# Kernel tuning notes

Hardware: AMD Instinct MI355X
Metric: run time of the kernel (lower is better)

## Reference

```python
import jax, jax.numpy as jnp
import numpy as np

N_EXPERTS = 8
TOPK = 2
D_MODEL = 1024
D_FF = 4096

def setup_inputs() -> dict:
    key = jax.random.key(0)
    k_x, k_g, k_1, k_2 = jax.random.split(key, 4)
    x = jax.random.normal(k_x, (4, 2048, D_MODEL), dtype=jnp.float32)
    Wg = jax.random.normal(k_g, (D_MODEL, N_EXPERTS), dtype=jnp.float32) * 0.02
    W1 = jax.random.normal(k_1, (N_EXPERTS, D_MODEL, D_FF), dtype=jnp.float32) * 0.02
    W2 = jax.random.normal(k_2, (N_EXPERTS, D_FF, D_MODEL), dtype=jnp.float32) * 0.02
    return {"x": x, "Wg": Wg, "W1": W1, "W2": W2}

def reference(x, Wg, W1, W2):
    B, S, D = x.shape
    xt = x.reshape(-1, D)                      # [T, D]
    T = xt.shape[0]
    logits = xt @ Wg                            # [T, E]
    vals, idx = jax.lax.top_k(logits, TOPK)     # [T, K]
    w = jax.nn.softmax(vals, axis=-1)           # renormalize over selected experts
    # scatter top-k weights into dense [T, E] gate matrix (zeros elsewhere)
    gates = jnp.zeros((T, N_EXPERTS), dtype=x.dtype).at[jnp.arange(T)[:, None], idx].set(w)
    out = jnp.zeros_like(xt)
    for e in range(N_EXPERTS):                  # fixed small loop over experts
        h = jax.nn.silu(xt @ W1[e]) @ W2[e]     # [T, D]
        out = out + gates[:, e:e+1] * h
    return out.reshape(B, S, D)
```

## Files before the change

kernel.cpp:

```cpp
#include <hip/hip_runtime.h>
#include <hip/hip_bf16.h>
#include <math.h>

#define T_TOK 8192
#define DM 1024
#define DF 4096
#define NE 8
#define MAXT 72

typedef __attribute__((ext_vector_type(4))) float  f32x4;
typedef __attribute__((ext_vector_type(8))) short  s16x8;
typedef __attribute__((ext_vector_type(8))) unsigned short u16x8;
typedef __attribute__((ext_vector_type(4))) unsigned short u16x4;

__device__ __forceinline__ unsigned short f2bf(float f) {
    unsigned int u = __builtin_bit_cast(unsigned int, f);
    u = (u + 0x7FFFu + ((u >> 16) & 1u)) >> 16;
    return (unsigned short)u;
}

#define GLDS16(gptr, lptr)                                                         \
    __builtin_amdgcn_global_load_lds(                                              \
        (const __attribute__((address_space(1))) void*)(gptr),                     \
        (__attribute__((address_space(3))) void*)(lptr), 16, 0, 0)

#define BAR() asm volatile("s_barrier" ::: "memory")

template<int W>
__device__ __forceinline__ void waitvm() {
    if constexpr (W == 6)      asm volatile("s_waitcnt vmcnt(6)" ::: "memory");
    else if constexpr (W == 3) asm volatile("s_waitcnt vmcnt(3)" ::: "memory");
    else                       asm volatile("s_waitcnt vmcnt(0)" ::: "memory");
}

__global__ __launch_bounds__(256) void route_kernel(
    const float* __restrict__ x, const float* __restrict__ Wg,
    int* __restrict__ counts, int* __restrict__ lists, float* __restrict__ pw,
    unsigned short* __restrict__ xb)
{
    int tok  = (int)((blockIdx.x * blockDim.x + threadIdx.x) >> 6);
    int lane = threadIdx.x & 63;
    if (tok >= T_TOK) return;

    const float* xr = x + (size_t)tok * DM;
    float acc[NE];
#pragma unroll
    for (int e = 0; e < NE; ++e) acc[e] = 0.f;

    for (int i = lane; i < DM; i += 64) {
        float xv = xr[i];
        const float* wr = Wg + (size_t)i * NE;
#pragma unroll
        for (int e = 0; e < NE; ++e) acc[e] += xv * wr[e];
    }

    if (xb) {
        unsigned short* xrow = xb + (size_t)tok * DM;
#pragma unroll
        for (int i = lane * 4; i < DM; i += 256) {
            float4 v = *reinterpret_cast<const float4*>(xr + i);
            u16x4 o;
            o[0] = f2bf(v.x); o[1] = f2bf(v.y); o[2] = f2bf(v.z); o[3] = f2bf(v.w);
            *reinterpret_cast<u16x4*>(xrow + i) = o;
        }
    }

#pragma unroll
    for (int e = 0; e < NE; ++e) {
#pragma unroll
        for (int off = 32; off > 0; off >>= 1)
            acc[e] += __shfl_xor(acc[e], off, 64);
    }

    if (lane == 0) {
        int i0 = 0; float v0 = acc[0];
#pragma unroll
        for (int e = 1; e < NE; ++e) if (acc[e] > v0) { v0 = acc[e]; i0 = e; }
        int i1 = -1; float v1 = -INFINITY;
#pragma unroll
        for (int e = 0; e < NE; ++e) if (e != i0 && acc[e] > v1) { v1 = acc[e]; i1 = e; }
        float e1 = __expf(v1 - v0);
        float s  = 1.f + e1;
        int p0 = tok * 2, p1 = tok * 2 + 1;
        pw[p0] = 1.f / s;
        pw[p1] = e1 / s;
        int pos0 = atomicAdd(&counts[i0], 1);
        lists[i0 * T_TOK + pos0] = p0;
        int pos1 = atomicAdd(&counts[i1], 1);
        lists[i1 * T_TOK + pos1] = p1;
    }
}

__global__ void offsets_kernel(const int* __restrict__ counts, int* __restrict__ offsets,
                               unsigned* __restrict__ table, int* __restrict__ ntp)
{
    if (threadIdx.x == 0) {
        int s = 0, ti = 0;
        for (int e = 0; e < NE; ++e) {
            offsets[e] = s;
            int cnt = counts[e];
            for (int t0 = 0; t0 < cnt; t0 += 256)
                table[ti++] = ((unsigned)e << 20) | (unsigned)t0;
            s += cnt;
        }
        ntp[0] = ti;
        for (; ti < MAXT; ++ti) table[ti] = 0xFFFFFFFFu;
    }
}

template<int K, int N>
__global__ __launch_bounds__(256) void transpose_conv_kernel(
    const float* __restrict__ W, unsigned short* __restrict__ Wt)
{
    int e  = blockIdx.z;
    int k0 = blockIdx.x * 64;
    int n0 = blockIdx.y * 64;
    const float* We = W + (size_t)e * K * N;
    unsigned short* Wte = Wt + (size_t)e * K * N;

    __shared__ unsigned short t[64][73];
    int c4 = (threadIdx.x & 15) * 4;
    int r  = threadIdx.x >> 4;
#pragma unroll
    for (int i = 0; i < 4; ++i) {
        int rr = r + i * 16;
        float4 v = *reinterpret_cast<const float4*>(We + (size_t)(k0 + rr) * N + n0 + c4);
        t[rr][c4 + 0] = f2bf(v.x); t[rr][c4 + 1] = f2bf(v.y);
        t[rr][c4 + 2] = f2bf(v.z); t[rr][c4 + 3] = f2bf(v.w);
    }
    __syncthreads();
    int kc = (threadIdx.x & 7) * 8;
    int rn = threadIdx.x >> 3;
#pragma unroll
    for (int i = 0; i < 2; ++i) {
        int nn = rn + i * 32;
        u16x8 o;
#pragma unroll
        for (int j = 0; j < 8; ++j) o[j] = t[kc + j][nn];
        *reinterpret_cast<u16x8*>(Wte + (size_t)(n0 + nn) * K + k0 + kc) = o;
    }
}

template<int N, int K, int SPLITK, bool IS_G1>
__global__ __launch_bounds__(512, 4) void moe_gemm11(
    const unsigned short* __restrict__ A,
    const unsigned short* __restrict__ Wt,
    const int* __restrict__ counts, const int* __restrict__ offsets,
    const int* __restrict__ lists, const unsigned* __restrict__ table,
    const int* __restrict__ ntp, const float* __restrict__ pw,
    unsigned short* __restrict__ Hout, float* __restrict__ Oout)
{
    constexpr int NT  = N / 128;
    constexpr int PAN = NT * SPLITK;
    constexpr int KS  = K / SPLITK;
    constexpr int NC  = KS / 32;
    static_assert(NC >= 4, "pipeline depth");

    __shared__ __attribute__((aligned(16))) char lds[73728];

    int ntl  = ntp[0];
    int live = ntl * PAN;
    int orig = blockIdx.x;
    if (orig >= live) return;
    int q = live >> 3, r = live & 7;
    int xq = orig & 7, ib = orig >> 3;
    int work = (xq < r ? xq * (q + 1) : r * (q + 1) + (xq - r) * q) + ib;
    int rt    = work / PAN;
    int panel = work - rt * PAN;
    int nt    = panel >> (SPLITK - 1);
    int sk    = panel & (SPLITK - 1);
    int koff  = sk * KS;

    unsigned te = table[rt];
    int e     = (int)(te >> 20);
    int slot0 = (int)(te & 0xFFFFFu);
    int cnt   = counts[e];
    int off   = offsets[e];
    int ntile = nt * 128;

    int tid  = threadIdx.x;
    int lane = tid & 63;
    int wid  = tid >> 6;
    int wm = wid >> 1;
    int wn = wid & 1;
    int l15 = lane & 15, l4 = lane >> 4;

    const unsigned short* Be = Wt + (size_t)e * N * K;

    int ssw = ((tid & 3) ^ ((tid >> 3) & 3)) * 8;
    unsigned aOff0, aOff1, bOff;
    {
        int r0 = tid >> 2;
#pragma unroll
        for (int u = 0; u < 2; ++u) {
            int sl = slot0 + u * 128 + r0;
            unsigned grow;
            if (IS_G1) grow = (sl < cnt) ? (unsigned)(lists[e * T_TOK + sl] >> 1) : 0u;
            else       grow = (unsigned)(off + ((sl < cnt) ? sl : slot0));
            unsigned v = grow * (unsigned)K + (unsigned)(koff + ssw);
            if (u == 0) aOff0 = v; else aOff1 = v;
        }
        bOff = (unsigned)(ntile + r0) * (unsigned)K + (unsigned)(koff + ssw);
    }

    auto stage = [&](int s, int c) {
        int ko = c * 32;
        char* dA = lds + s * 16384 + tid * 16;
        char* dB = lds + 49152 + s * 8192 + tid * 16;
        GLDS16(A + aOff0 + ko, dA);
        GLDS16(A + aOff1 + ko, dA + 8192);
        GLDS16(Be + bOff + ko, dB);
    };

    int swzb = (l4 ^ ((l15 >> 1) & 3)) * 16;
    int aRd = (wm * 64 + l15) * 64 + swzb;
    int bRd = (wn * 64 + l15) * 64 + swzb;

    f32x4 acc[4][4];
#pragma unroll
    for (int m = 0; m < 4; ++m)
#pragma unroll
        for (int n = 0; n < 4; ++n) acc[m][n] = (f32x4){0.f, 0.f, 0.f, 0.f};

    auto compute = [&](int s) {
        const char* Ab = lds + s * 16384;
        const char* Bb = lds + 49152 + s * 8192;
        s16x8 af[4];
#pragma unroll
        for (int m = 0; m < 4; ++m)
            af[m] = *reinterpret_cast<const s16x8*>(Ab + aRd + m * 1024);
        __builtin_amdgcn_s_setprio(1);
#pragma unroll
        for (int n = 0; n < 4; ++n) {
            s16x8 bf = *reinterpret_cast<const s16x8*>(Bb + bRd + n * 1024);
#pragma unroll
            for (int m = 0; m < 4; ++m)
                acc[m][n] = __builtin_amdgcn_mfma_f32_16x16x32_bf16(af[m], bf, acc[m][n], 0, 0, 0);
        }
        __builtin_amdgcn_s_setprio(0);
    };

    stage(0, 0); stage(1, 1); stage(2, 2);
    int sslot = 0;
    for (int c = 0; c < NC; ++c) {
        if (c + 2 < NC)      waitvm<6>();
        else if (c + 1 < NC) waitvm<3>();
        else                 waitvm<0>();
        BAR();
        compute(sslot);
        BAR();
        if (c + 3 < NC) stage(sslot, c + 3);
        sslot = (sslot == 2) ? 0 : sslot + 1;
    }

#pragma unroll
    for (int m = 0; m < 4; ++m) {
        int trow = wm * 64 + m * 16 + l4 * 4;
#pragma unroll
        for (int rr = 0; rr < 4; ++rr) {
            int slot = slot0 + trow + rr;
            if (slot >= cnt) continue;
            if (IS_G1) {
                unsigned short* hr = Hout + (size_t)(off + slot) * N;
#pragma unroll
                for (int n = 0; n < 4; ++n) {
                    int col = ntile + wn * 64 + n * 16 + l15;
                    float v = acc[m][n][rr];
                    float s = v / (1.f + __expf(-v));
                    hr[col] = f2bf(s);
                }
            } else {
                int p = lists[e * T_TOK + slot];
                float w = pw[p];
                float* orow = Oout + (size_t)(p >> 1) * DM;
#pragma unroll
                for (int n = 0; n < 4; ++n) {
                    int col = ntile + wn * 64 + n * 16 + l15;
                    atomicAdd(orow + col, w * acc[m][n][rr]);
                }
            }
        }
    }
}

#define BMF 16
#define BFF 256
__global__ __launch_bounds__(256) void expert_gemm_f32(
    const float* __restrict__ x, const float* __restrict__ W1, const float* __restrict__ W2,
    const int* __restrict__ counts, const int* __restrict__ lists, const float* __restrict__ pw,
    float* __restrict__ out)
{
    int e    = blockIdx.y;
    int tile = blockIdx.x;
    int cnt  = counts[e];
    int start = tile * BMF;
    if (start >= cnt) return;

    __shared__ float xs[BMF][DM];
    __shared__ float hs[BMF][BFF];
    __shared__ int   toks[BMF];
    __shared__ float wgt[BMF];

    int tid = threadIdx.x;
    int nm  = cnt - start; if (nm > BMF) nm = BMF;

    if (tid < BMF) {
        if (tid < nm) {
            int p = lists[e * T_TOK + start + tid];
            toks[tid] = p >> 1;
            wgt[tid]  = pw[p];
        } else { toks[tid] = -1; wgt[tid] = 0.f; }
    }
    __syncthreads();
    for (int m = 0; m < BMF; ++m) {
        int t = toks[m];
        const float* xr = (t >= 0) ? (x + (size_t)t * DM) : nullptr;
        for (int i = tid; i < DM; i += 256) xs[m][i] = (t >= 0) ? xr[i] : 0.f;
    }
    __syncthreads();

    const float* W1e = W1 + (size_t)e * DM * DF;
    const float* W2e = W2 + (size_t)e * DF * DM;
    float acc[BMF][4];
#pragma unroll
    for (int m = 0; m < BMF; ++m)
#pragma unroll
        for (int c = 0; c < 4; ++c) acc[m][c] = 0.f;

    for (int fc = 0; fc < DF; fc += BFF) {
        float hacc[BMF];
#pragma unroll
        for (int m = 0; m < BMF; ++m) hacc[m] = 0.f;
        const float* w1col = W1e + fc + tid;
#pragma unroll 4
        for (int i = 0; i < DM; ++i) {
            float w1v = w1col[(size_t)i * DF];
#pragma unroll
            for (int m = 0; m < BMF; ++m) hacc[m] += xs[m][i] * w1v;
        }
        __syncthreads();
#pragma unroll
        for (int m = 0; m < BMF; ++m) {
            float v = hacc[m];
            hs[m][tid] = v / (1.f + __expf(-v));
        }
        __syncthreads();
        const float* w2base = W2e + (size_t)fc * DM + tid * 4;
        for (int f = 0; f < BFF; ++f) {
            float4 w2v = *reinterpret_cast<const float4*>(w2base + (size_t)f * DM);
#pragma unroll
            for (int m = 0; m < BMF; ++m) {
                float h = hs[m][f];
                acc[m][0] += h * w2v.x; acc[m][1] += h * w2v.y;
                acc[m][2] += h * w2v.z; acc[m][3] += h * w2v.w;
            }
        }
        __syncthreads();
    }
    int c0 = tid * 4;
#pragma unroll
    for (int m = 0; m < BMF; ++m) {
        int t = toks[m];
        if (t < 0) continue;
        float w = wgt[m];
        float* op = out + (size_t)t * DM + c0;
        atomicAdd(op + 0, w * acc[m][0]);
        atomicAdd(op + 1, w * acc[m][1]);
        atomicAdd(op + 2, w * acc[m][2]);
        atomicAdd(op + 3, w * acc[m][3]);
    }
}

extern "C" void kernel_launch(void* const* d_in, const int* in_sizes, int n_in,
                              void* d_out, int out_size, void* d_ws, size_t ws_size,
                              hipStream_t stream)
{
    const float* x  = (const float*)d_in[0];
    const float* Wg = (const float*)d_in[1];
    const float* W1 = (const float*)d_in[2];
    const float* W2 = (const float*)d_in[3];
    float* out = (float*)d_out;

    char* ws = (char*)d_ws;
    int*      counts  = (int*)(ws + 0);
    int*      offsets = (int*)(ws + 64);
    int*      ntp     = (int*)(ws + 128);
    unsigned* table   = (unsigned*)(ws + 256);
    int*      lists   = (int*)(ws + 2048);
    float*    pw      = (float*)(ws + 2048 + 262144);

    const size_t o_xb  = 524288;
    const size_t sz_xb = (size_t)T_TOK * DM * 2;
    const size_t o_w1t = o_xb + sz_xb;
    const size_t sz_w  = (size_t)NE * DM * DF * 2;
    const size_t o_w2t = o_w1t + sz_w;
    const size_t o_h   = o_w2t + sz_w;
    const size_t sz_h  = (size_t)(2 * T_TOK) * DF * 2;
    const size_t NEEDED = o_h + sz_h;

    bool fast = (ws_size >= NEEDED);
    unsigned short* xb = fast ? (unsigned short*)(ws + o_xb) : nullptr;

    hipMemsetAsync(counts, 0, 64, stream);
    route_kernel<<<T_TOK / 4, 256, 0, stream>>>(x, Wg, counts, lists, pw, xb);

    if (fast) {
        unsigned short* w1t = (unsigned short*)(ws + o_w1t);
        unsigned short* w2t = (unsigned short*)(ws + o_w2t);
        unsigned short* H   = (unsigned short*)(ws + o_h);

        hipMemsetAsync(d_out, 0, (size_t)out_size * sizeof(float), stream);
        offsets_kernel<<<1, 64, 0, stream>>>(counts, offsets, table, ntp);
        {
            dim3 g(DM / 64, DF / 64, NE);
            transpose_conv_kernel<DM, DF><<<g, 256, 0, stream>>>(W1, w1t);
        }
        {
            dim3 g(DF / 64, DM / 64, NE);
            transpose_conv_kernel<DF, DM><<<g, 256, 0, stream>>>(W2, w2t);
        }
        moe_gemm11<DF, DM, 1, true><<<dim3(MAXT * 32), 512, 0, stream>>>(
            xb, w1t, counts, offsets, lists, table, ntp, pw, H, nullptr);
        moe_gemm11<DM, DF, 2, false><<<dim3(MAXT * 16), 512, 0, stream>>>(
            H, w2t, counts, offsets, lists, table, ntp, pw, nullptr, out);
    } else {
        hipMemsetAsync(d_out, 0, (size_t)out_size * sizeof(float), stream);
        dim3 grid(T_TOK / BMF, NE);
        expert_gemm_f32<<<grid, 256, 0, stream>>>(x, W1, W2, counts, lists, pw, out);
    }
}
```

Baseline: 695.3 us.

## Fold output zeroing into routing, merge transposes, compute expert tiles in GEMM

Zeroes the output buffer inside the routing kernel instead of a separate memset, merges the two weight transpose/convert kernels into one launch, and removes the offsets kernel by having each GEMM block rebuild the tile table from the expert counts. The routing dot product is also vectorized with float4 loads, reusing the x loads for the bf16 conversion. This cuts several launches and a redundant pass over x, in exchange for a small amount of redundant per-block scalar work in the GEMMs.

```diff
diff --git a/kernel.cpp b/kernel.cpp
--- a/kernel.cpp
+++ b/kernel.cpp
@@ -36,31 +36,45 @@
 __global__ __launch_bounds__(256) void route_kernel(
     const float* __restrict__ x, const float* __restrict__ Wg,
     int* __restrict__ counts, int* __restrict__ lists, float* __restrict__ pw,
-    unsigned short* __restrict__ xb)
+    unsigned short* __restrict__ xb, float* __restrict__ outz)
 {
+    {
+        size_t base = ((size_t)blockIdx.x * 256 + threadIdx.x) * 16;
+        float4 z = {0.f, 0.f, 0.f, 0.f};
+#pragma unroll
+        for (int j = 0; j < 4; ++j)
+            *reinterpret_cast<float4*>(outz + base + j * 4) = z;
+    }
+
     int tok  = (int)((blockIdx.x * blockDim.x + threadIdx.x) >> 6);
     int lane = threadIdx.x & 63;
     if (tok >= T_TOK) return;
 
     const float* xr = x + (size_t)tok * DM;
+    unsigned short* xrow = xb ? (xb + (size_t)tok * DM) : nullptr;
+
     float acc[NE];
 #pragma unroll
     for (int e = 0; e < NE; ++e) acc[e] = 0.f;
 
-    for (int i = lane; i < DM; i += 64) {
-        float xv = xr[i];
-        const float* wr = Wg + (size_t)i * NE;
-#pragma unroll
-        for (int e = 0; e < NE; ++e) acc[e] += xv * wr[e];
-    }
-
-    if (xb) {
-        unsigned short* xrow = xb + (size_t)tok * DM;
-#pragma unroll
-        for (int i = lane * 4; i < DM; i += 256) {
-            float4 v = *reinterpret_cast<const float4*>(xr + i);
+#pragma unroll
+    for (int s = 0; s < 4; ++s) {
+        int i = s * 256 + lane * 4;
+        float4 xv = *reinterpret_cast<const float4*>(xr + i);
+#pragma unroll
+        for (int j = 0; j < 4; ++j) {
+            const float* wr = Wg + (size_t)(i + j) * NE;
+            float4 w0 = *reinterpret_cast<const float4*>(wr);
+            float4 w1 = *reinterpret_cast<const float4*>(wr + 4);
+            float xs = (j == 0) ? xv.x : (j == 1) ? xv.y : (j == 2) ? xv.z : xv.w;
+            acc[0] += xs * w0.x; acc[1] += xs * w0.y;
+            acc[2] += xs * w0.z; acc[3] += xs * w0.w;
+            acc[4] += xs * w1.x; acc[5] += xs * w1.y;
+            acc[6] += xs * w1.z; acc[7] += xs * w1.w;
+        }
+        if (xrow) {
             u16x4 o;
-            o[0] = f2bf(v.x); o[1] = f2bf(v.y); o[2] = f2bf(v.z); o[3] = f2bf(v.w);
+            o[0] = f2bf(xv.x); o[1] = f2bf(xv.y); o[2] = f2bf(xv.z); o[3] = f2bf(xv.w);
             *reinterpret_cast<u16x4*>(xrow + i) = o;
         }
     }
@@ -91,39 +105,31 @@
     }
 }
 
-__global__ void offsets_kernel(const int* __restrict__ counts, int* __restrict__ offsets,
-                               unsigned* __restrict__ table, int* __restrict__ ntp)
+__global__ __launch_bounds__(256) void transpose_conv_all(
+    const float* __restrict__ W1, const float* __restrict__ W2,
+    unsigned short* __restrict__ w1t, unsigned short* __restrict__ w2t)
 {
-    if (threadIdx.x == 0) {
-        int s = 0, ti = 0;
-        for (int e = 0; e < NE; ++e) {
-            offsets[e] = s;
-            int cnt = counts[e];
-            for (int t0 = 0; t0 < cnt; t0 += 256)
-                table[ti++] = ((unsigned)e << 20) | (unsigned)t0;
-            s += cnt;
-        }
-        ntp[0] = ti;
-        for (; ti < MAXT; ++ti) table[ti] = 0xFFFFFFFFu;
-    }
-}
-
-template<int K, int N>
-__global__ __launch_bounds__(256) void transpose_conv_kernel(
-    const float* __restrict__ W, unsigned short* __restrict__ Wt)
-{
-    int e  = blockIdx.z;
-    int k0 = blockIdx.x * 64;
-    int n0 = blockIdx.y * 64;
+    int id = blockIdx.x;
+    const float* W; unsigned short* Wt; int K, N, e, k0, n0;
+    if (id < 8192) {
+        W = W1; Wt = w1t; K = DM; N = DF;
+        e = id >> 10; int r = id & 1023;
+        k0 = (r & 15) * 64; n0 = (r >> 4) * 64;
+    } else {
+        id -= 8192;
+        W = W2; Wt = w2t; K = DF; N = DM;
+        e = id >> 10; int r = id & 1023;
+        k0 = (r >> 4) * 64; n0 = (r & 15) * 64;
+    }
     const float* We = W + (size_t)e * K * N;
     unsigned short* Wte = Wt + (size_t)e * K * N;
 
     __shared__ unsigned short t[64][73];
     int c4 = (threadIdx.x & 15) * 4;
-    int r  = threadIdx.x >> 4;
+    int rr0 = threadIdx.x >> 4;
 #pragma unroll
     for (int i = 0; i < 4; ++i) {
-        int rr = r + i * 16;
+        int rr = rr0 + i * 16;
         float4 v = *reinterpret_cast<const float4*>(We + (size_t)(k0 + rr) * N + n0 + c4);
         t[rr][c4 + 0] = f2bf(v.x); t[rr][c4 + 1] = f2bf(v.y);
         t[rr][c4 + 2] = f2bf(v.z); t[rr][c4 + 3] = f2bf(v.w);
@@ -142,12 +148,11 @@
 }
 
 template<int N, int K, int SPLITK, bool IS_G1>
-__global__ __launch_bounds__(512, 4) void moe_gemm11(
+__global__ __launch_bounds__(512, 4) void moe_gemm14(
     const unsigned short* __restrict__ A,
     const unsigned short* __restrict__ Wt,
-    const int* __restrict__ counts, const int* __restrict__ offsets,
-    const int* __restrict__ lists, const unsigned* __restrict__ table,
-    const int* __restrict__ ntp, const float* __restrict__ pw,
+    const int* __restrict__ counts, const int* __restrict__ lists,
+    const float* __restrict__ pw,
     unsigned short* __restrict__ Hout, float* __restrict__ Oout)
 {
     constexpr int NT  = N / 128;
@@ -158,7 +163,13 @@
 
     __shared__ __attribute__((aligned(16))) char lds[73728];
 
-    int ntl  = ntp[0];
+    int cnts[NE];
+#pragma unroll
+    for (int i = 0; i < NE; ++i) cnts[i] = counts[i];
+    int ntl = 0;
+#pragma unroll
+    for (int i = 0; i < NE; ++i) ntl += (cnts[i] + 255) >> 8;
+
     int live = ntl * PAN;
     int orig = blockIdx.x;
     if (orig >= live) return;
@@ -171,11 +182,17 @@
     int sk    = panel & (SPLITK - 1);
     int koff  = sk * KS;
 
-    unsigned te = table[rt];
-    int e     = (int)(te >> 20);
-    int slot0 = (int)(te & 0xFFFFFu);
-    int cnt   = counts[e];
-    int off   = offsets[e];
+    int e = 0, tb = 0, off = 0, cnt = 0;
+    {
+        int ctb = 0, cob = 0; bool found = false;
+#pragma unroll
+        for (int i = 0; i < NE; ++i) {
+            int ti = (cnts[i] + 255) >> 8;
+            if (!found && rt < ctb + ti) { e = i; tb = ctb; off = cob; cnt = cnts[i]; found = true; }
+            ctb += ti; cob += cnts[i];
+        }
+    }
+    int slot0 = (rt - tb) << 8;
     int ntile = nt * 128;
 
     int tid  = threadIdx.x;
@@ -383,9 +400,6 @@
 
     char* ws = (char*)d_ws;
     int*      counts  = (int*)(ws + 0);
-    int*      offsets = (int*)(ws + 64);
-    int*      ntp     = (int*)(ws + 128);
-    unsigned* table   = (unsigned*)(ws + 256);
     int*      lists   = (int*)(ws + 2048);
     float*    pw      = (float*)(ws + 2048 + 262144);
 
@@ -402,29 +416,19 @@
     unsigned short* xb = fast ? (unsigned short*)(ws + o_xb) : nullptr;
 
     hipMemsetAsync(counts, 0, 64, stream);
-    route_kernel<<<T_TOK / 4, 256, 0, stream>>>(x, Wg, counts, lists, pw, xb);
+    route_kernel<<<T_TOK / 4, 256, 0, stream>>>(x, Wg, counts, lists, pw, xb, out);
 
     if (fast) {
         unsigned short* w1t = (unsigned short*)(ws + o_w1t);
         unsigned short* w2t = (unsigned short*)(ws + o_w2t);
         unsigned short* H   = (unsigned short*)(ws + o_h);
 
-        hipMemsetAsync(d_out, 0, (size_t)out_size * sizeof(float), stream);
-        offsets_kernel<<<1, 64, 0, stream>>>(counts, offsets, table, ntp);
-        {
-            dim3 g(DM / 64, DF / 64, NE);
-            transpose_conv_kernel<DM, DF><<<g, 256, 0, stream>>>(W1, w1t);
-        }
-        {
-            dim3 g(DF / 64, DM / 64, NE);
-            transpose_conv_kernel<DF, DM><<<g, 256, 0, stream>>>(W2, w2t);
-        }
-        moe_gemm11<DF, DM, 1, true><<<dim3(MAXT * 32), 512, 0, stream>>>(
-            xb, w1t, counts, offsets, lists, table, ntp, pw, H, nullptr);
-        moe_gemm11<DM, DF, 2, false><<<dim3(MAXT * 16), 512, 0, stream>>>(
-            H, w2t, counts, offsets, lists, table, ntp, pw, nullptr, out);
+        transpose_conv_all<<<16384, 256, 0, stream>>>(W1, W2, w1t, w2t);
+        moe_gemm14<DF, DM, 1, true><<<dim3(MAXT * 32), 512, 0, stream>>>(
+            xb, w1t, counts, lists, pw, H, nullptr);
+        moe_gemm14<DM, DF, 2, false><<<dim3(MAXT * 16), 512, 0, stream>>>(
+            H, w2t, counts, lists, pw, nullptr, out);
     } else {
-        hipMemsetAsync(d_out, 0, (size_t)out_size * sizeof(float), stream);
         dim3 grid(T_TOK / BMF, NE);
         expert_gemm_f32<<<grid, 256, 0, stream>>>(x, W1, W2, counts, lists, pw, out);
     }
```

Result: faster. 675.8 us (-2.8%).
